# Kernel optimization log

Hardware: AMD Instinct MI355X
Metric: run time of the kernel (lower is better)

## Reference

```python
import jax, jax.numpy as jnp
import numpy as np

D, E, DFF, TOPK = 768, 4, 1024, 2


def setup_inputs() -> dict:
    key = jax.random.key(0)
    ks = jax.random.split(key, 6)
    s = 0.02  # init scale for weights
    return {
        "input_ids": jax.random.normal(ks[0], (8, 2048, D), dtype=jnp.float32),
        "W": jax.random.normal(ks[1], (D, D), dtype=jnp.float32) * s,
        "b": jnp.zeros((D,), dtype=jnp.float32),
        "Wg": jax.random.normal(ks[2], (D, E), dtype=jnp.float32) * s,
        "bg": jnp.zeros((E,), dtype=jnp.float32),
        "W1": jax.random.normal(ks[3], (E, D, DFF), dtype=jnp.float32) * s,
        "b1": jnp.zeros((E, DFF), dtype=jnp.float32),
        "W2": jax.random.normal(ks[4], (E, DFF, D), dtype=jnp.float32) * s,
        "b2": jnp.zeros((E, D), dtype=jnp.float32),
    }


def reference(input_ids, W, b, Wg, bg, W1, b1, W2, b2):
    B, S, _ = input_ids.shape
    # Dense projection feeding the MoE layer
    h = jnp.einsum("bsd,de->bse", input_ids, W) + b          # [B,S,D]
    t = h.reshape(-1, D)                                      # [T,D] tokens

    # Token-choice router: softmax over experts, top-2, renormalized gates
    logits = t @ Wg + bg                                      # [T,E]
    probs = jax.nn.softmax(logits, axis=-1)
    vals, idx = jax.lax.top_k(probs, TOPK)                    # [T,K]
    gates = vals / jnp.sum(vals, axis=-1, keepdims=True)
    # Dense combine weights [T,E]: zero for non-selected experts
    comb = jnp.sum(jax.nn.one_hot(idx, E, dtype=t.dtype) * gates[..., None], axis=1)

    # Expert FFNs (E small -> compute all experts, weighted combine)
    pre = jnp.einsum("td,edf->etf", t, W1) + b1[:, None, :]   # [E,T,DFF]
    y_e = jnp.einsum("etf,efd->etd", jax.nn.gelu(pre), W2) + b2[:, None, :]
    out = jnp.einsum("te,etd->td", comb, y_e)                 # [T,D]
    return out.reshape(B, S, D)
```

## Files before the change

kernel.cpp:

```cpp
#include <hip/hip_runtime.h>

#define DIM 768
#define NEXP 4
#define DFF_ 1024
#define CAP 16384

typedef __attribute__((ext_vector_type(4))) float f32x4;
typedef __attribute__((ext_vector_type(8))) short s16x8;

__device__ __forceinline__ unsigned short f32_to_bf16(float f) {
  unsigned int u = __float_as_uint(f);
  unsigned int r = (u + 0x7FFFu + ((u >> 16) & 1u)) >> 16;
  return (unsigned short)r;
}
__device__ __forceinline__ float bf16_to_f32(unsigned short u) {
  return __uint_as_float(((unsigned int)u) << 16);
}

__global__ void transpose_bf16_kernel(const float* __restrict__ in,
                                      unsigned short* __restrict__ out,
                                      int R, int C, int ldo, int zOut) {
  __shared__ float tile[32][33];
  const int bx = blockIdx.x, by = blockIdx.y, bz = blockIdx.z;
  in  += (size_t)bz * R * C;
  out += (size_t)bz * zOut;
  const int tx = threadIdx.x, ty = threadIdx.y;
#pragma unroll
  for (int i = 0; i < 4; i++) {
    int r = by * 32 + ty + i * 8;
    int c = bx * 32 + tx;
    tile[ty + i * 8][tx] = in[(size_t)r * C + c];
  }
  __syncthreads();
#pragma unroll
  for (int i = 0; i < 4; i++) {
    int oc = bx * 32 + ty + i * 8;
    int orow = by * 32 + tx;
    out[(size_t)oc * ldo + orow] = f32_to_bf16(tile[tx][ty + i * 8]);
  }
}

__global__ void convert_bf16_kernel(const float* __restrict__ in,
                                    unsigned short* __restrict__ out) {
  size_t i = ((size_t)blockIdx.x * 256 + threadIdx.x) * 8;
  float4 a = *(const float4*)(in + i);
  float4 b = *(const float4*)(in + i + 4);
  union { unsigned short u[8]; uint4 v; } pk;
  pk.u[0] = f32_to_bf16(a.x); pk.u[1] = f32_to_bf16(a.y);
  pk.u[2] = f32_to_bf16(a.z); pk.u[3] = f32_to_bf16(a.w);
  pk.u[4] = f32_to_bf16(b.x); pk.u[5] = f32_to_bf16(b.y);
  pk.u[6] = f32_to_bf16(b.z); pk.u[7] = f32_to_bf16(b.w);
  *(uint4*)(out + i) = pk.v;
}

__global__ void wfg_kernel(const float* __restrict__ W, const float* __restrict__ Wg,
                           const float* __restrict__ b, const float* __restrict__ bg,
                           float* __restrict__ wfg, float* __restrict__ bgp) {
  int gid = blockIdx.x * 256 + threadIdx.x;
  if (gid < DIM * NEXP) {
    int k = gid >> 2, e = gid & 3;
    const float* wr = W + (size_t)k * DIM;
    float acc = 0.f;
    for (int d = 0; d < DIM; d++) acc += wr[d] * Wg[d * NEXP + e];
    wfg[gid] = acc;
  } else if (gid < DIM * NEXP + NEXP) {
    int e = gid - DIM * NEXP;
    float acc = bg[e];
    for (int d = 0; d < DIM; d++) acc += b[d] * Wg[d * NEXP + e];
    bgp[e] = acc;
  }
}

__global__ void router_kernel(const float* __restrict__ x, const float* __restrict__ wfg,
                              const float* __restrict__ bgp,
                              int2* __restrict__ rte, float2* __restrict__ rtg) {
  __shared__ float wfgS[DIM * NEXP];
  const int tid = threadIdx.x;
  for (int i = tid; i < DIM * NEXP; i += 256) wfgS[i] = wfg[i];
  __syncthreads();
  const int w = tid >> 6, lane = tid & 63;
  const size_t t = (size_t)blockIdx.x * 4 + w;
  const float* xr = x + t * DIM;
  float a0 = 0.f, a1 = 0.f, a2 = 0.f, a3 = 0.f;
#pragma unroll
  for (int i = 0; i < 12; i++) {
    int k = i * 64 + lane;
    float xv = xr[k];
    a0 += xv * wfgS[k * 4 + 0];
    a1 += xv * wfgS[k * 4 + 1];
    a2 += xv * wfgS[k * 4 + 2];
    a3 += xv * wfgS[k * 4 + 3];
  }
#pragma unroll
  for (int off = 32; off > 0; off >>= 1) {
    a0 += __shfl_xor(a0, off);
    a1 += __shfl_xor(a1, off);
    a2 += __shfl_xor(a2, off);
    a3 += __shfl_xor(a3, off);
  }
  if (lane == 0) {
    float l[NEXP] = {a0 + bgp[0], a1 + bgp[1], a2 + bgp[2], a3 + bgp[3]};
    float m = fmaxf(fmaxf(l[0], l[1]), fmaxf(l[2], l[3]));
    float p[NEXP]; float s = 0.f;
#pragma unroll
    for (int e = 0; e < NEXP; e++) { p[e] = expf(l[e] - m); s += p[e]; }
#pragma unroll
    for (int e = 0; e < NEXP; e++) p[e] /= s;
    int i1 = 0;
#pragma unroll
    for (int e = 1; e < NEXP; e++) if (p[e] > p[i1]) i1 = e;
    int i2 = -1;
#pragma unroll
    for (int e = 0; e < NEXP; e++) { if (e == i1) continue; if (i2 < 0 || p[e] > p[i2]) i2 = e; }
    float denom = p[i1] + p[i2];
    rte[t] = make_int2(i1, i2);
    rtg[t] = make_float2(p[i1] / denom, p[i2] / denom);
  }
}

__global__ void assign_kernel(const int2* __restrict__ rte, const float2* __restrict__ rtg,
                              int* __restrict__ cnt, int* __restrict__ idx_tok,
                              float* __restrict__ gate_sel, int2* __restrict__ tok_slot) {
  __shared__ int hist[NEXP];
  __shared__ int base[NEXP];
  const int tid = threadIdx.x;
  if (tid < NEXP) hist[tid] = 0;
  __syncthreads();
  const int t = blockIdx.x * 256 + tid;
  int2 e = rte[t];
  float2 g = rtg[t];
  int r1 = atomicAdd(&hist[e.x], 1);
  int r2 = atomicAdd(&hist[e.y], 1);
  __syncthreads();
  if (tid < NEXP) base[tid] = atomicAdd(&cnt[tid], hist[tid]);
  __syncthreads();
  int s1 = base[e.x] + r1, s2 = base[e.y] + r2;
  idx_tok[e.x * CAP + s1] = t;  gate_sel[e.x * CAP + s1] = g.x;
  idx_tok[e.y * CAP + s2] = t;  gate_sel[e.y * CAP + s2] = g.y;
  tok_slot[t] = make_int2((e.x << 14) | s1, (e.y << 14) | s2);
}

__global__ void combine_kernel(const unsigned short* __restrict__ y,
                               const int2* __restrict__ tok_slot,
                               const float2* __restrict__ rtg,
                               const int* __restrict__ cnts,
                               const float* __restrict__ b2,
                               float* __restrict__ out) {
  __shared__ float b2S[NEXP * DIM];
  const int tid = threadIdx.x;
  for (int i = tid; i < NEXP * DIM; i += 256) b2S[i] = b2[i];
  const int t0 = (cnts[0] + 127) >> 7, t1 = (cnts[1] + 127) >> 7, t2 = (cnts[2] + 127) >> 7;
  const int rb[NEXP] = {0, t0 * 128, (t0 + t1) * 128, (t0 + t1 + t2) * 128};
  __syncthreads();
  const int w = tid >> 6, lane = tid & 63;
  const size_t t = (size_t)blockIdx.x * 4 + w;
  int2 v = tok_slot[t];
  float2 cg = rtg[t];
  const int e1 = v.x >> 14, s1 = v.x & (CAP - 1);
  const int e2 = v.y >> 14, s2 = v.y & (CAP - 1);
  const unsigned short* y1 = y + (size_t)(rb[e1] + s1) * DIM;
  const unsigned short* y2 = y + (size_t)(rb[e2] + s2) * DIM;
  float* op = out + t * DIM;
  const float* bp1 = b2S + e1 * DIM;
  const float* bp2 = b2S + e2 * DIM;
#pragma unroll
  for (int k = 0; k < 12; k++) {
    int n = k * 64 + lane;
    op[n] = bf16_to_f32(y1[n]) + bf16_to_f32(y2[n]) + cg.x * bp1[n] + cg.y * bp2[n];
  }
}

template <int MODE, int CH>
__launch_bounds__(256)
__global__ void gemm_kernel(const unsigned short* __restrict__ A, const int lda,
                            const unsigned short* __restrict__ Bt, const int ldb,
                            const int K, const int N,
                            const float* __restrict__ bias,
                            const int* __restrict__ idx_tok,
                            const float* __restrict__ gate_sel,
                            const int* __restrict__ cnts,
                            unsigned short* __restrict__ outB, const int ldo) {
  const int lin = blockIdx.y * gridDim.x + blockIdx.x;
  const int nT = gridDim.x;
  const int xcd = lin & 7, t8 = lin >> 3;
  int bn = 0, bm0 = 0;
  int bmLoc = 0, cnt = 1 << 30, segBase = 0, gRow0 = 0;

  if constexpr (MODE == 0) {
    const int perXcd = gridDim.y >> 3;
    const int mi = t8 % CH;
    const int rest = t8 / CH;
    bn = rest % nT;
    const int mc = rest / nT;
    bm0 = (xcd * perXcd + mc * CH + mi) * 128;
  } else {
    const int c0 = cnts[0], c1 = cnts[1], c2 = cnts[2], c3 = cnts[3];
    const int t0 = (c0 + 127) >> 7, t1 = (c1 + 127) >> 7,
              t2 = (c2 + 127) >> 7, t3 = (c3 + 127) >> 7;
    const int p1 = t0, p2 = p1 + t1, p3 = p2 + t2, tot = p3 + t3;
    const int perXcd = (tot + 7) >> 3;
    bn = t8 % nT;
    const int mloc = t8 / nT;
    if (mloc >= perXcd) return;
    const int mIdx = xcd * perXcd + mloc;
    if (mIdx >= tot) return;
    const int seg = (mIdx >= p2) ? ((mIdx >= p3) ? 3 : 2) : ((mIdx >= p1) ? 1 : 0);
    const int pre = (seg == 3) ? p3 : (seg == 2) ? p2 : (seg == 1) ? p1 : 0;
    bmLoc = (mIdx - pre) * 128;
    segBase = seg * CAP;
    gRow0 = mIdx * 128;
    cnt = (seg == 3) ? c3 : (seg == 2) ? c2 : (seg == 1) ? c1 : c0;
    Bt += (size_t)seg * N * ldb;
    if constexpr (MODE == 1) bias += (size_t)seg * N;
  }

  __shared__ unsigned short As[128 * 32];
  __shared__ unsigned short Bs[128 * 32];
  __shared__ int idxS[128];
  __shared__ float gateS[128];

  const int tid = threadIdx.x;
  const int w = tid >> 6;
  const int lane = tid & 63;

  if constexpr (MODE == 1) {
    if (tid < 128) {
      int r = bmLoc + tid;
      int cl = (r < cnt) ? r : bmLoc;
      idxS[tid] = idx_tok[segBase + cl];
      gateS[tid] = gate_sel[segBase + cl];
    }
    __syncthreads();
  }

  const int r0 = tid >> 2, r1 = 64 + r0;
  const int gq = (tid & 3) ^ (r0 & 3);
  const unsigned short *aP0, *aP1;
  if constexpr (MODE == 0) {
    aP0 = A + (size_t)(bm0 + r0) * lda + gq * 8;
    aP1 = A + (size_t)(bm0 + r1) * lda + gq * 8;
  } else if constexpr (MODE == 1) {
    aP0 = A + (size_t)idxS[r0] * lda + gq * 8;
    aP1 = A + (size_t)idxS[r1] * lda + gq * 8;
  } else {
    aP0 = A + (size_t)(gRow0 + r0) * lda + gq * 8;
    aP1 = A + (size_t)(gRow0 + r1) * lda + gq * 8;
  }
  const unsigned short* bP0 = Bt + (size_t)(bn * 128 + r0) * ldb + gq * 8;
  const unsigned short* bP1 = Bt + (size_t)(bn * 128 + r1) * ldb + gq * 8;

  f32x4 acc[4][4];
#pragma unroll
  for (int i = 0; i < 4; i++)
#pragma unroll
    for (int j = 0; j < 4; j++) acc[i][j] = (f32x4){0.f, 0.f, 0.f, 0.f};

  const int quad = lane >> 4;
  const int m16 = lane & 15;
  const int wm = (w & 1) * 64;
  const int wn = (w >> 1) * 64;

  for (int k0 = 0; k0 < K; k0 += 32) {
    char* la0 = (char*)As + w * 1024;
    char* la1 = (char*)As + 4096 + w * 1024;
    char* lb0 = (char*)Bs + w * 1024;
    char* lb1 = (char*)Bs + 4096 + w * 1024;
    __builtin_amdgcn_global_load_lds((const __attribute__((address_space(1))) void*)(aP0 + k0),
                                     (__attribute__((address_space(3))) void*)la0, 16, 0, 0);
    __builtin_amdgcn_global_load_lds((const __attribute__((address_space(1))) void*)(aP1 + k0),
                                     (__attribute__((address_space(3))) void*)la1, 16, 0, 0);
    __builtin_amdgcn_global_load_lds((const __attribute__((address_space(1))) void*)(bP0 + k0),
                                     (__attribute__((address_space(3))) void*)lb0, 16, 0, 0);
    __builtin_amdgcn_global_load_lds((const __attribute__((address_space(1))) void*)(bP1 + k0),
                                     (__attribute__((address_space(3))) void*)lb1, 16, 0, 0);
    __syncthreads();
    const int sw = (quad ^ (m16 & 3)) * 16;
    s16x8 af[4], bf[4];
#pragma unroll
    for (int i = 0; i < 4; i++)
      af[i] = *(const s16x8*)((const char*)As + (wm + i * 16 + m16) * 64 + sw);
#pragma unroll
    for (int j = 0; j < 4; j++)
      bf[j] = *(const s16x8*)((const char*)Bs + (wn + j * 16 + m16) * 64 + sw);
#pragma unroll
    for (int i = 0; i < 4; i++)
#pragma unroll
      for (int j = 0; j < 4; j++)
        acc[i][j] = __builtin_amdgcn_mfma_f32_16x16x32_bf16(af[i], bf[j], acc[i][j], 0, 0, 0);
    __syncthreads();
  }

#pragma unroll
  for (int i = 0; i < 4; i++) {
    const int rloc = wm + i * 16 + quad * 4;
#pragma unroll
    for (int j = 0; j < 4; j++) {
      const int col = bn * 128 + wn + j * 16 + m16;
      if constexpr (MODE == 0) {
        float bv = bias[col];
#pragma unroll
        for (int r = 0; r < 4; r++)
          outB[(size_t)(bm0 + rloc + r) * ldo + col] = f32_to_bf16(acc[i][j][r] + bv);
      } else if constexpr (MODE == 1) {
        float bv = bias[col];
#pragma unroll
        for (int r = 0; r < 4; r++) {
          if (bmLoc + rloc + r < cnt) {
            float v = acc[i][j][r] + bv;
            float t3 = v + 0.044715f * v * v * v;
            float e2 = exp2f(t3 * 2.302208206984525f);
            float rc = __builtin_amdgcn_rcpf(1.0f + e2);
            float g = v - v * rc;
            outB[(size_t)(gRow0 + rloc + r) * ldo + col] = f32_to_bf16(g * gateS[rloc + r]);
          }
        }
      } else {
#pragma unroll
        for (int r = 0; r < 4; r++) {
          if (bmLoc + rloc + r < cnt)
            outB[(size_t)(gRow0 + rloc + r) * ldo + col] = f32_to_bf16(acc[i][j][r]);
        }
      }
    }
  }
}

extern "C" void kernel_launch(void* const* d_in, const int* in_sizes, int n_in,
                              void* d_out, int out_size, void* d_ws, size_t ws_size,
                              hipStream_t stream) {
  (void)in_sizes; (void)n_in; (void)out_size; (void)ws_size;
  const float* x  = (const float*)d_in[0];
  const float* W  = (const float*)d_in[1];
  const float* b  = (const float*)d_in[2];
  const float* Wg = (const float*)d_in[3];
  const float* bg = (const float*)d_in[4];
  const float* W1 = (const float*)d_in[5];
  const float* b1 = (const float*)d_in[6];
  const float* W2 = (const float*)d_in[7];
  const float* b2 = (const float*)d_in[8];
  float* out = (float*)d_out;
  char* ws = (char*)d_ws;

  unsigned short* tbf  = (unsigned short*)(ws + 0);
  unsigned short* w1t  = (unsigned short*)(ws + 25165824);
  unsigned short* w2t  = (unsigned short*)(ws + 31457280);
  float* wfg           = (float*)(ws + 37748736);
  float* bgp           = (float*)(ws + 37761024);
  int2*  rte           = (int2*)(ws + 37761280);
  float2* rtg          = (float2*)(ws + 37892352);
  int*   cnt           = (int*)(ws + 38023424);
  int*   idx_tok       = (int*)(ws + 38023680);
  float* gate_sel      = (float*)(ws + 38285824);
  int2*  tok_slot      = (int2*)(ws + 38547968);
  unsigned short* g    = (unsigned short*)(ws + 38679040);
  unsigned short* xbf  = (unsigned short*)(ws + 38679040);
  unsigned short* wt   = (unsigned short*)(ws + 63844864);
  unsigned short* y    = (unsigned short*)(ws + 106574336);

  hipMemsetAsync(cnt, 0, NEXP * sizeof(int), stream);
  transpose_bf16_kernel<<<dim3(24, 24, 1), dim3(32, 8), 0, stream>>>(W, wt, 768, 768, 768, 589824);
  transpose_bf16_kernel<<<dim3(32, 24, 4), dim3(32, 8), 0, stream>>>(W1, w1t, 768, 1024, 768, 786432);
  transpose_bf16_kernel<<<dim3(24, 32, 4), dim3(32, 8), 0, stream>>>(W2, w2t, 1024, 768, 1024, 786432);
  convert_bf16_kernel<<<6144, 256, 0, stream>>>(x, xbf);
  wfg_kernel<<<13, 256, 0, stream>>>(W, Wg, b, bg, wfg, bgp);
  router_kernel<<<4096, 256, 0, stream>>>(x, wfg, bgp, rte, rtg);
  assign_kernel<<<64, 256, 0, stream>>>(rte, rtg, cnt, idx_tok, gate_sel, tok_slot);

  gemm_kernel<0, 8><<<dim3(6, 128), 256, 0, stream>>>(
      xbf, 768, wt, 768, 768, 768, b, nullptr, nullptr, nullptr, tbf, 768);
  gemm_kernel<1, 8><<<dim3(8, 264), 256, 0, stream>>>(
      tbf, 768, w1t, 768, 768, 1024, b1, idx_tok, gate_sel, cnt, g, 1024);
  gemm_kernel<2, 8><<<dim3(6, 264), 256, 0, stream>>>(
      g, 1024, w2t, 1024, 1024, 768, nullptr, nullptr, nullptr, cnt, y, 768);
  combine_kernel<<<4096, 256, 0, stream>>>(y, tok_slot, rtg, cnt, b2, out);
}
```

Baseline: 429.8 us.

## Double-buffer GEMM LDS tiles and fuse bf16 input conversion into router

The GEMM main loop now uses two LDS buffers for each operand, so the next K tile is fetched with global_load_lds while MFMAs run on the current one, and only one barrier remains per iteration. The separate convert_bf16 kernel is removed and the router kernel writes the bf16 copy of x while it reads x for the gating dot products, saving one full read of the fp32 input and one launch. The cost is doubled LDS use per block, which may lower occupancy. Correctness relies on the async LDS loads finishing before the next iteration's barrier.

Measured after the change: 422.3 us. Within noise of the previous version (-1.7%).

```diff
diff --git a/kernel.cpp b/kernel.cpp
--- a/kernel.cpp
+++ b/kernel.cpp
@@ -38,19 +38,6 @@
     int orow = by * 32 + tx;
     out[(size_t)oc * ldo + orow] = f32_to_bf16(tile[tx][ty + i * 8]);
   }
-}
-
-__global__ void convert_bf16_kernel(const float* __restrict__ in,
-                                    unsigned short* __restrict__ out) {
-  size_t i = ((size_t)blockIdx.x * 256 + threadIdx.x) * 8;
-  float4 a = *(const float4*)(in + i);
-  float4 b = *(const float4*)(in + i + 4);
-  union { unsigned short u[8]; uint4 v; } pk;
-  pk.u[0] = f32_to_bf16(a.x); pk.u[1] = f32_to_bf16(a.y);
-  pk.u[2] = f32_to_bf16(a.z); pk.u[3] = f32_to_bf16(a.w);
-  pk.u[4] = f32_to_bf16(b.x); pk.u[5] = f32_to_bf16(b.y);
-  pk.u[6] = f32_to_bf16(b.z); pk.u[7] = f32_to_bf16(b.w);
-  *(uint4*)(out + i) = pk.v;
 }
 
 __global__ void wfg_kernel(const float* __restrict__ W, const float* __restrict__ Wg,
@@ -73,7 +60,8 @@
 
 __global__ void router_kernel(const float* __restrict__ x, const float* __restrict__ wfg,
                               const float* __restrict__ bgp,
-                              int2* __restrict__ rte, float2* __restrict__ rtg) {
+                              int2* __restrict__ rte, float2* __restrict__ rtg,
+                              unsigned short* __restrict__ xbf) {
   __shared__ float wfgS[DIM * NEXP];
   const int tid = threadIdx.x;
   for (int i = tid; i < DIM * NEXP; i += 256) wfgS[i] = wfg[i];
@@ -81,15 +69,20 @@
   const int w = tid >> 6, lane = tid & 63;
   const size_t t = (size_t)blockIdx.x * 4 + w;
   const float* xr = x + t * DIM;
+  unsigned short* xbr = xbf + t * DIM;
   float a0 = 0.f, a1 = 0.f, a2 = 0.f, a3 = 0.f;
 #pragma unroll
-  for (int i = 0; i < 12; i++) {
-    int k = i * 64 + lane;
-    float xv = xr[k];
-    a0 += xv * wfgS[k * 4 + 0];
-    a1 += xv * wfgS[k * 4 + 1];
-    a2 += xv * wfgS[k * 4 + 2];
-    a3 += xv * wfgS[k * 4 + 3];
+  for (int i = 0; i < 6; i++) {
+    int k = i * 128 + lane * 2;
+    float2 xv = *(const float2*)(xr + k);
+    ushort2 pk;
+    pk.x = f32_to_bf16(xv.x);
+    pk.y = f32_to_bf16(xv.y);
+    *(ushort2*)(xbr + k) = pk;
+    a0 += xv.x * wfgS[k * 4 + 0] + xv.y * wfgS[k * 4 + 4];
+    a1 += xv.x * wfgS[k * 4 + 1] + xv.y * wfgS[k * 4 + 5];
+    a2 += xv.x * wfgS[k * 4 + 2] + xv.y * wfgS[k * 4 + 6];
+    a3 += xv.x * wfgS[k * 4 + 3] + xv.y * wfgS[k * 4 + 7];
   }
 #pragma unroll
   for (int off = 32; off > 0; off >>= 1) {
@@ -214,8 +207,8 @@
     if constexpr (MODE == 1) bias += (size_t)seg * N;
   }
 
-  __shared__ unsigned short As[128 * 32];
-  __shared__ unsigned short Bs[128 * 32];
+  __shared__ unsigned short As[2][128 * 32];
+  __shared__ unsigned short Bs[2][128 * 32];
   __shared__ int idxS[128];
   __shared__ float gateS[128];
 
@@ -249,6 +242,22 @@
   const unsigned short* bP0 = Bt + (size_t)(bn * 128 + r0) * ldb + gq * 8;
   const unsigned short* bP1 = Bt + (size_t)(bn * 128 + r1) * ldb + gq * 8;
 
+#define ISSUE(bufi, kk)                                                                        \
+  {                                                                                            \
+    char* la0 = (char*)As[bufi] + w * 1024;                                                    \
+    char* la1 = (char*)As[bufi] + 4096 + w * 1024;                                             \
+    char* lb0 = (char*)Bs[bufi] + w * 1024;                                                    \
+    char* lb1 = (char*)Bs[bufi] + 4096 + w * 1024;                                             \
+    __builtin_amdgcn_global_load_lds((const __attribute__((address_space(1))) void*)(aP0 + (kk)), \
+                                     (__attribute__((address_space(3))) void*)la0, 16, 0, 0);  \
+    __builtin_amdgcn_global_load_lds((const __attribute__((address_space(1))) void*)(aP1 + (kk)), \
+                                     (__attribute__((address_space(3))) void*)la1, 16, 0, 0);  \
+    __builtin_amdgcn_global_load_lds((const __attribute__((address_space(1))) void*)(bP0 + (kk)), \
+                                     (__attribute__((address_space(3))) void*)lb0, 16, 0, 0);  \
+    __builtin_amdgcn_global_load_lds((const __attribute__((address_space(1))) void*)(bP1 + (kk)), \
+                                     (__attribute__((address_space(3))) void*)lb1, 16, 0, 0);  \
+  }
+
   f32x4 acc[4][4];
 #pragma unroll
   for (int i = 0; i < 4; i++)
@@ -259,36 +268,30 @@
   const int m16 = lane & 15;
   const int wm = (w & 1) * 64;
   const int wn = (w >> 1) * 64;
-
+  const int sw = (quad ^ (m16 & 3)) * 16;
+
+  ISSUE(0, 0);
+  int buf = 0;
   for (int k0 = 0; k0 < K; k0 += 32) {
-    char* la0 = (char*)As + w * 1024;
-    char* la1 = (char*)As + 4096 + w * 1024;
-    char* lb0 = (char*)Bs + w * 1024;
-    char* lb1 = (char*)Bs + 4096 + w * 1024;
-    __builtin_amdgcn_global_load_lds((const __attribute__((address_space(1))) void*)(aP0 + k0),
-                                     (__attribute__((address_space(3))) void*)la0, 16, 0, 0);
-    __builtin_amdgcn_global_load_lds((const __attribute__((address_space(1))) void*)(aP1 + k0),
-                                     (__attribute__((address_space(3))) void*)la1, 16, 0, 0);
-    __builtin_amdgcn_global_load_lds((const __attribute__((address_space(1))) void*)(bP0 + k0),
-                                     (__attribute__((address_space(3))) void*)lb0, 16, 0, 0);
-    __builtin_amdgcn_global_load_lds((const __attribute__((address_space(1))) void*)(bP1 + k0),
-                                     (__attribute__((address_space(3))) void*)lb1, 16, 0, 0);
     __syncthreads();
-    const int sw = (quad ^ (m16 & 3)) * 16;
-    s16x8 af[4], bf[4];
+    if (k0 + 32 < K) ISSUE(buf ^ 1, k0 + 32);
+    const char* Ab = (const char*)As[buf];
+    const char* Bb = (const char*)Bs[buf];
+    s16x8 af[4], bf4[4];
 #pragma unroll
     for (int i = 0; i < 4; i++)
-      af[i] = *(const s16x8*)((const char*)As + (wm + i * 16 + m16) * 64 + sw);
+      af[i] = *(const s16x8*)(Ab + (wm + i * 16 + m16) * 64 + sw);
 #pragma unroll
     for (int j = 0; j < 4; j++)
-      bf[j] = *(const s16x8*)((const char*)Bs + (wn + j * 16 + m16) * 64 + sw);
+      bf4[j] = *(const s16x8*)(Bb + (wn + j * 16 + m16) * 64 + sw);
 #pragma unroll
     for (int i = 0; i < 4; i++)
 #pragma unroll
       for (int j = 0; j < 4; j++)
-        acc[i][j] = __builtin_amdgcn_mfma_f32_16x16x32_bf16(af[i], bf[j], acc[i][j], 0, 0, 0);
-    __syncthreads();
-  }
+        acc[i][j] = __builtin_amdgcn_mfma_f32_16x16x32_bf16(af[i], bf4[j], acc[i][j], 0, 0, 0);
+    buf ^= 1;
+  }
+#undef ISSUE
 
 #pragma unroll
   for (int i = 0; i < 4; i++) {
@@ -361,9 +364,8 @@
   transpose_bf16_kernel<<<dim3(24, 24, 1), dim3(32, 8), 0, stream>>>(W, wt, 768, 768, 768, 589824);
   transpose_bf16_kernel<<<dim3(32, 24, 4), dim3(32, 8), 0, stream>>>(W1, w1t, 768, 1024, 768, 786432);
   transpose_bf16_kernel<<<dim3(24, 32, 4), dim3(32, 8), 0, stream>>>(W2, w2t, 1024, 768, 1024, 786432);
-  convert_bf16_kernel<<<6144, 256, 0, stream>>>(x, xbf);
   wfg_kernel<<<13, 256, 0, stream>>>(W, Wg, b, bg, wfg, bgp);
-  router_kernel<<<4096, 256, 0, stream>>>(x, wfg, bgp, rte, rtg);
+  router_kernel<<<4096, 256, 0, stream>>>(x, wfg, bgp, rte, rtg, xbf);
   assign_kernel<<<64, 256, 0, stream>>>(rte, rtg, cnt, idx_tok, gate_sel, tok_slot);
 
   gemm_kernel<0, 8><<<dim3(6, 128), 256, 0, stream>>>(
```
